# Performance work log

Measured on AMD Instinct MI355X. Metric: run time of the kernel, lower is better.

## Reference

```python
import jax, jax.numpy as jnp
import numpy as np

N, E, D_IN, D_OUT = 50000, 800000, 128, 128
LN_EPS = 1e-5


def setup_inputs() -> dict:
    key = jax.random.key(0)
    ks = jax.random.split(key, 7)
    x = jax.random.normal(ks[0], (N, D_IN), dtype=jnp.float32)
    adj = jax.random.randint(ks[1], (2, E), 0, N, dtype=jnp.int32)  # edge_index
    scale = 1.0 / np.sqrt(D_IN)
    W_gcn = jax.random.normal(ks[2], (D_IN, D_OUT), dtype=jnp.float32) * scale
    b_gcn = jax.random.normal(ks[3], (D_OUT,), dtype=jnp.float32) * 0.02
    W_lin = jax.random.normal(ks[4], (D_IN, D_OUT), dtype=jnp.float32) * scale
    ln_w = jnp.ones((D_OUT,), dtype=jnp.float32)
    ln_b = jnp.zeros((D_OUT,), dtype=jnp.float32)
    return {"adj": adj, "x": x, "W_gcn": W_gcn, "b_gcn": b_gcn,
            "W_lin": W_lin, "ln_w": ln_w, "ln_b": ln_b}


def _gcn_conv(x, edge_index, W, b):
    """PyG GCNConv: add self-loops, symmetric D^-1/2 (A+I) D^-1/2 normalization."""
    n = x.shape[0]
    loop = jnp.arange(n, dtype=edge_index.dtype)
    src = jnp.concatenate([edge_index[0], loop])  # message sources (x_j)
    dst = jnp.concatenate([edge_index[1], loop])  # aggregation targets
    ones = jnp.ones(src.shape[0], dtype=x.dtype)
    deg = jax.ops.segment_sum(ones, dst, num_segments=n)
    dinv = jnp.where(deg > 0, jax.lax.rsqrt(deg), 0.0)
    norm = dinv[src] * dinv[dst]                   # [E+N]
    h = x @ W                                      # [N, D_OUT] project first (PyG order)
    msg = h[src] * norm[:, None]                   # gather + scale
    agg = jax.ops.segment_sum(msg, dst, num_segments=n)
    return agg + b


def _layer_norm(y, w, b):
    mu = jnp.mean(y, axis=-1, keepdims=True)
    var = jnp.mean(jnp.square(y - mu), axis=-1, keepdims=True)
    return (y - mu) * jax.lax.rsqrt(var + LN_EPS) * w + b


def reference(adj, x, W_gcn, b_gcn, W_lin, ln_w, ln_b):
    x1 = _gcn_conv(x, adj, W_gcn, b_gcn)
    x2 = x @ W_lin                                  # bias=False linear
    return _layer_norm(x1 + x2 + 1e-6, ln_w, ln_b)
```

## Files before the change

kernel.cpp:

```cpp
#include <hip/hip_runtime.h>
#include <hip/hip_bf16.h>

#define NN 50000
#define EE 800000
#define DD 128
#define CB 196
#define EBLK 2048
#define NEB 391

typedef __attribute__((ext_vector_type(8))) short bf16x8;
typedef __attribute__((ext_vector_type(4))) float f32x4;

static __device__ __forceinline__ unsigned short f2bf(float f) {
  union { float f; unsigned u; } v; v.f = f;
  unsigned r = v.u + 0x7FFFu + ((v.u >> 16) & 1u);
  return (unsigned short)(r >> 16);
}
static __device__ __forceinline__ float bf2f(unsigned short h) {
  union { unsigned u; float f; } v; v.u = ((unsigned)h) << 16;
  return v.f;
}

__global__ __launch_bounds__(256) void k_p0(
    const int* __restrict__ dst, int* __restrict__ coarseCnt,
    const float* __restrict__ Wg, const float* __restrict__ Wl,
    unsigned short* __restrict__ Wt, const float4* __restrict__ x4,
    ushort4* __restrict__ xb4) {
  int b = blockIdx.x, t = threadIdx.x;
  if (b < NEB) {
    __shared__ int cnt[CB];
    for (int i = t; i < CB; i += 256) cnt[i] = 0;
    __syncthreads();
    int e0 = b * EBLK;
    for (int i = t; i < EBLK; i += 256) {
      int e = e0 + i;
      if (e < EE) atomicAdd(&cnt[dst[e] >> 8], 1);
    }
    __syncthreads();
    for (int i = t; i < CB; i += 256)
      if (cnt[i]) atomicAdd(&coarseCnt[i], cnt[i]);
  } else if (b < NEB + 32) {
    for (int i = (b - NEB) * 256 + t; i < DD * 256; i += 32 * 256) {
      int n = i >> 8, k = i & 255;
      float v = (k < 128) ? Wg[k * DD + n] : Wl[(k - 128) * DD + n];
      Wt[i] = f2bf(v);
    }
  } else {
    int base = (b - NEB - 32) * 1024 + t;
#pragma unroll
    for (int k = 0; k < 4; k++) {
      int i = base + k * 256;
      if (i < NN * 32) {
        float4 v = x4[i];
        ushort4 o;
        o.x = f2bf(v.x); o.y = f2bf(v.y); o.z = f2bf(v.z); o.w = f2bf(v.w);
        xb4[i] = o;
      }
    }
  }
}

__global__ __launch_bounds__(256) void k_pscan(const int* __restrict__ coarseCnt,
                                               int* __restrict__ coarseStart,
                                               int* __restrict__ cursor) {
  __shared__ int s[256];
  int t = threadIdx.x;
  int v = (t < CB) ? coarseCnt[t] : 0;
  s[t] = v;
  for (int off = 1; off < 256; off <<= 1) {
    __syncthreads();
    int tmp = (t >= off) ? s[t - off] : 0;
    __syncthreads();
    if (t >= off) s[t] += tmp;
  }
  __syncthreads();
  if (t < CB) {
    coarseStart[t] = s[t] - v;
    cursor[t] = s[t] - v;
  }
}

__global__ __launch_bounds__(256) void k_p1a(const int* __restrict__ src,
                                             const int* __restrict__ dst,
                                             int* __restrict__ cursor,
                                             unsigned int* __restrict__ pairs) {
  __shared__ unsigned int stage[EBLK];
  __shared__ int cnt[CB], base_[CB], cur[CB];
  int t = threadIdx.x;
  int e0 = blockIdx.x * EBLK;
  for (int i = t; i < CB; i += 256) { cnt[i] = 0; cur[i] = 0; }
  __syncthreads();
  for (int i = t; i < EBLK; i += 256) {
    int e = e0 + i;
    unsigned int p = 0xFFFFFFFFu;
    if (e < EE) {
      int d = dst[e], s = src[e];
      int cb = d >> 8;
      p = (unsigned int)s | ((unsigned int)(d & 255) << 16) | ((unsigned int)cb << 24);
      atomicAdd(&cnt[cb], 1);
    }
    stage[i] = p;
  }
  __syncthreads();
  for (int i = t; i < CB; i += 256)
    base_[i] = cnt[i] ? atomicAdd(&cursor[i], cnt[i]) : 0;
  __syncthreads();
  for (int i = t; i < EBLK; i += 256) {
    unsigned int p = stage[i];
    if (p != 0xFFFFFFFFu) {
      int cb = p >> 24;
      int ofs = atomicAdd(&cur[cb], 1);
      pairs[base_[cb] + ofs] = p;
    }
  }
}

__global__ __launch_bounds__(512) void k_p1b(
    const unsigned int* __restrict__ pairs, const int* __restrict__ coarseStart,
    const int* __restrict__ coarseCnt, const unsigned short* __restrict__ xb,
    int* __restrict__ deg, float* __restrict__ dinv, int* __restrict__ rowStart,
    unsigned short* __restrict__ srcU16, unsigned short* __restrict__ xs) {
  __shared__ int ldeg[256], lscan[256], lcur[256];
  __shared__ float ldinvs[256];
  int cb = blockIdx.x, t = threadIdx.x;
  int start = coarseStart[cb], cnt = coarseCnt[cb];
  int n0 = cb << 8;
  int nloc = NN - n0; if (nloc > 256) nloc = 256;
  if (t < 256) ldeg[t] = 0;
  __syncthreads();
  for (int i = t; i < cnt; i += 512)
    atomicAdd(&ldeg[(pairs[start + i] >> 16) & 255], 1);
  __syncthreads();
  if (t < 256) lscan[t] = ldeg[t];
  for (int off = 1; off < 256; off <<= 1) {
    __syncthreads();
    int tmp = (t >= off && t < 256) ? lscan[t - off] : 0;
    __syncthreads();
    if (t >= off && t < 256) lscan[t] += tmp;
  }
  __syncthreads();
  if (t < 256) {
    int dg = ldeg[t];
    int rs = start + lscan[t] - dg;
    lcur[t] = rs;
    float di = rsqrtf((float)(dg + 1));
    ldinvs[t] = di;
    if (t < nloc) { deg[n0 + t] = dg; dinv[n0 + t] = di; rowStart[n0 + t] = rs; }
  }
  __syncthreads();
  for (int i = t; i < cnt; i += 512) {
    unsigned int pr = pairs[start + i];
    int pos = atomicAdd(&lcur[(pr >> 16) & 255], 1);
    srcU16[pos] = (unsigned short)(pr & 0xFFFFu);
  }
  for (int i = t; i < nloc * 16; i += 512) {
    int rr = i >> 4, q = i & 15;
    bf16x8 v = *(const bf16x8*)(xb + (size_t)(n0 + rr) * DD + q * 8);
    float di = ldinvs[rr];
    bf16x8 o;
#pragma unroll
    for (int k = 0; k < 8; k++) o[k] = (short)f2bf(bf2f((unsigned short)v[k]) * di);
    *(bf16x8*)(xs + (size_t)(n0 + rr) * DD + q * 8) = o;
  }
}

__global__ __launch_bounds__(256) void k_agg2(
    const unsigned short* __restrict__ xs, const int* __restrict__ rowStart,
    const int* __restrict__ deg, const unsigned short* __restrict__ srcU16,
    const float* __restrict__ dinv, unsigned short* __restrict__ agg) {
  int t = threadIdx.x;
  int g = t >> 4, r = t & 15;
  int node = blockIdx.x * 16 + g;
  int lane = t & 63;
  int srcLaneBase = lane & 48;
  float acc[8];
  {
    bf16x8 vs = *(const bf16x8*)(xs + (size_t)node * DD + r * 8);
#pragma unroll
    for (int k = 0; k < 8; k++) acc[k] = bf2f((unsigned short)vs[k]);
  }
  int js = rowStart[node], cnt = deg[node];
  for (int base = 0; base < cnt; base += 16) {
    int idx = (base + r < cnt) ? (int)srcU16[js + base + r] : 0;
    int m = cnt - base; if (m > 16) m = 16;
    int j = 0;
    for (; j + 8 <= m; j += 8) {
      int s0 = __shfl(idx, srcLaneBase + j);
      int s1 = __shfl(idx, srcLaneBase + j + 1);
      int s2 = __shfl(idx, srcLaneBase + j + 2);
      int s3 = __shfl(idx, srcLaneBase + j + 3);
      int s4 = __shfl(idx, srcLaneBase + j + 4);
      int s5 = __shfl(idx, srcLaneBase + j + 5);
      int s6 = __shfl(idx, srcLaneBase + j + 6);
      int s7 = __shfl(idx, srcLaneBase + j + 7);
      bf16x8 v0 = *(const bf16x8*)(xs + (size_t)s0 * DD + r * 8);
      bf16x8 v1 = *(const bf16x8*)(xs + (size_t)s1 * DD + r * 8);
      bf16x8 v2 = *(const bf16x8*)(xs + (size_t)s2 * DD + r * 8);
      bf16x8 v3 = *(const bf16x8*)(xs + (size_t)s3 * DD + r * 8);
      bf16x8 v4 = *(const bf16x8*)(xs + (size_t)s4 * DD + r * 8);
      bf16x8 v5 = *(const bf16x8*)(xs + (size_t)s5 * DD + r * 8);
      bf16x8 v6 = *(const bf16x8*)(xs + (size_t)s6 * DD + r * 8);
      bf16x8 v7 = *(const bf16x8*)(xs + (size_t)s7 * DD + r * 8);
#pragma unroll
      for (int k = 0; k < 8; k++) acc[k] += bf2f((unsigned short)v0[k]);
#pragma unroll
      for (int k = 0; k < 8; k++) acc[k] += bf2f((unsigned short)v1[k]);
#pragma unroll
      for (int k = 0; k < 8; k++) acc[k] += bf2f((unsigned short)v2[k]);
#pragma unroll
      for (int k = 0; k < 8; k++) acc[k] += bf2f((unsigned short)v3[k]);
#pragma unroll
      for (int k = 0; k < 8; k++) acc[k] += bf2f((unsigned short)v4[k]);
#pragma unroll
      for (int k = 0; k < 8; k++) acc[k] += bf2f((unsigned short)v5[k]);
#pragma unroll
      for (int k = 0; k < 8; k++) acc[k] += bf2f((unsigned short)v6[k]);
#pragma unroll
      for (int k = 0; k < 8; k++) acc[k] += bf2f((unsigned short)v7[k]);
    }
    for (; j < m; j++) {
      int s = __shfl(idx, srcLaneBase + j);
      bf16x8 v = *(const bf16x8*)(xs + (size_t)s * DD + r * 8);
#pragma unroll
      for (int k = 0; k < 8; k++) acc[k] += bf2f((unsigned short)v[k]);
    }
  }
  float d = dinv[node];
  bf16x8 o;
#pragma unroll
  for (int k = 0; k < 8; k++) o[k] = (short)f2bf(acc[k] * d);
  *(bf16x8*)(agg + (size_t)node * DD + r * 8) = o;
}

__global__ __launch_bounds__(256) void k_mm_ln(
    const unsigned short* __restrict__ agg, const unsigned short* __restrict__ xb,
    const unsigned short* __restrict__ Wt, const float* __restrict__ bgcn,
    const float* __restrict__ lnw, const float* __restrict__ lnb,
    float* __restrict__ out) {
  int t = threadIdx.x;
  int w = t >> 6, lane = t & 63;
  int quad = lane >> 4, r = lane & 15;
  int m0 = (blockIdx.x * 4 + w) * 16;
  f32x4 zero = {0.f, 0.f, 0.f, 0.f};
  f32x4 acc[8];
#pragma unroll
  for (int i = 0; i < 8; i++) acc[i] = zero;
  int rowA = m0 + r;
  if (rowA > NN - 1) rowA = NN - 1;
#pragma unroll
  for (int ks = 0; ks < 8; ks++) {
    bf16x8 a;
    if (ks < 4) a = *(const bf16x8*)(agg + (size_t)rowA * DD + ks * 32 + quad * 8);
    else        a = *(const bf16x8*)(xb + (size_t)rowA * DD + (ks - 4) * 32 + quad * 8);
#pragma unroll
    for (int nt = 0; nt < 8; nt++) {
      bf16x8 b = *(const bf16x8*)(Wt + (size_t)(nt * 16 + r) * 256 + ks * 32 + quad * 8);
      acc[nt] = __builtin_amdgcn_mfma_f32_16x16x32_bf16(a, b, acc[nt], 0, 0, 0);
    }
  }
  float bg[8], lw[8], lb[8];
#pragma unroll
  for (int nt = 0; nt < 8; nt++) {
    int col = nt * 16 + r;
    bg[nt] = bgcn[col] + 1e-6f;
    lw[nt] = lnw[col];
    lb[nt] = lnb[col];
  }
#pragma unroll
  for (int reg = 0; reg < 4; reg++) {
    float y[8];
    float s1 = 0.f, s2 = 0.f;
#pragma unroll
    for (int nt = 0; nt < 8; nt++) {
      y[nt] = acc[nt][reg] + bg[nt];
      s1 += y[nt];
      s2 += y[nt] * y[nt];
    }
#pragma unroll
    for (int off = 1; off < 16; off <<= 1) {
      s1 += __shfl_xor(s1, off);
      s2 += __shfl_xor(s2, off);
    }
    float mu = s1 * (1.0f / 128.0f);
    float var = s2 * (1.0f / 128.0f) - mu * mu;
    float inv = rsqrtf(var + 1e-5f);
    int row = m0 + quad * 4 + reg;
    if (row < NN) {
#pragma unroll
      for (int nt = 0; nt < 8; nt++) {
        out[(size_t)row * DD + nt * 16 + r] = (y[nt] - mu) * inv * lw[nt] + lb[nt];
      }
    }
  }
}

extern "C" void kernel_launch(void* const* d_in, const int* in_sizes, int n_in,
                              void* d_out, int out_size, void* d_ws, size_t ws_size,
                              hipStream_t stream) {
  const int* adj = (const int*)d_in[0];
  const float* x = (const float*)d_in[1];
  const float* Wg = (const float*)d_in[2];
  const float* bg = (const float*)d_in[3];
  const float* Wl = (const float*)d_in[4];
  const float* lw = (const float*)d_in[5];
  const float* lb = (const float*)d_in[6];
  const int* srcp = adj;
  const int* dstp = adj + EE;
  float* out = (float*)d_out;

  char* ws = (char*)d_ws;
  size_t off = 0;
  auto alloc = [&](size_t bytes) -> void* {
    void* p = ws + off;
    off += (bytes + 255) & ~(size_t)255;
    return p;
  };
  int* coarseCnt = (int*)alloc((size_t)CB * 4);
  int* coarseStart = (int*)alloc((size_t)CB * 4);
  int* cursor = (int*)alloc((size_t)CB * 4);
  unsigned int* pairs = (unsigned int*)alloc((size_t)EE * 4);
  unsigned short* srcU16 = (unsigned short*)alloc((size_t)EE * 2);
  int* deg = (int*)alloc((size_t)NN * 4);
  float* dinv = (float*)alloc((size_t)NN * 4);
  int* rowStart = (int*)alloc((size_t)NN * 4);
  unsigned short* xb = (unsigned short*)alloc((size_t)NN * DD * 2);
  unsigned short* xs = (unsigned short*)alloc((size_t)NN * DD * 2);
  unsigned short* agg = (unsigned short*)alloc((size_t)NN * DD * 2);
  unsigned short* Wt = (unsigned short*)alloc((size_t)DD * 256 * 2);
  (void)ws_size; (void)in_sizes; (void)n_in; (void)out_size;

  hipMemsetAsync(coarseCnt, 0, (size_t)CB * 4, stream);
  k_p0<<<NEB + 32 + 1563, 256, 0, stream>>>(dstp, coarseCnt, Wg, Wl, Wt,
                                            (const float4*)x, (ushort4*)xb);
  k_pscan<<<1, 256, 0, stream>>>(coarseCnt, coarseStart, cursor);
  k_p1a<<<NEB, 256, 0, stream>>>(srcp, dstp, cursor, pairs);
  k_p1b<<<CB, 512, 0, stream>>>(pairs, coarseStart, coarseCnt, xb, deg, dinv,
                                rowStart, srcU16, xs);
  k_agg2<<<3125, 256, 0, stream>>>(xs, rowStart, deg, srcU16, dinv, agg);
  k_mm_ln<<<782, 256, 0, stream>>>(agg, xb, Wt, bg, lw, lb, out);
}
```

Before: 198.8 us.

## Fold coarse scan into partition kernels and count degrees with global atomics

Removes the single-block scan kernel. Each partition block now recomputes the coarse-bucket exclusive scan itself, and the per-node block derives its start offset from a reduction of earlier bucket counts. Node degrees are counted with global atomics in the first pass instead of a shared-memory histogram over pairs, and the edge block size is doubled to halve the block count. This saves one launch and a pass over pairs, at the cost of 800k global atomics on deg and redundant scans in every block.

```diff
diff --git a/kernel.cpp b/kernel.cpp
--- a/kernel.cpp
+++ b/kernel.cpp
@@ -5,8 +5,8 @@
 #define EE 800000
 #define DD 128
 #define CB 196
-#define EBLK 2048
-#define NEB 391
+#define EBLK 4096
+#define NEB 196
 
 typedef __attribute__((ext_vector_type(8))) short bf16x8;
 typedef __attribute__((ext_vector_type(4))) float f32x4;
@@ -23,6 +23,7 @@
 
 __global__ __launch_bounds__(256) void k_p0(
     const int* __restrict__ dst, int* __restrict__ coarseCnt,
+    int* __restrict__ deg,
     const float* __restrict__ Wg, const float* __restrict__ Wl,
     unsigned short* __restrict__ Wt, const float4* __restrict__ x4,
     ushort4* __restrict__ xb4) {
@@ -34,7 +35,11 @@
     int e0 = b * EBLK;
     for (int i = t; i < EBLK; i += 256) {
       int e = e0 + i;
-      if (e < EE) atomicAdd(&cnt[dst[e] >> 8], 1);
+      if (e < EE) {
+        int d = dst[e];
+        atomicAdd(&cnt[d >> 8], 1);
+        atomicAdd(&deg[d], 1);
+      }
     }
     __syncthreads();
     for (int i = t; i < CB; i += 256)
@@ -60,37 +65,21 @@
   }
 }
 
-__global__ __launch_bounds__(256) void k_pscan(const int* __restrict__ coarseCnt,
-                                               int* __restrict__ coarseStart,
-                                               int* __restrict__ cursor) {
-  __shared__ int s[256];
-  int t = threadIdx.x;
-  int v = (t < CB) ? coarseCnt[t] : 0;
-  s[t] = v;
-  for (int off = 1; off < 256; off <<= 1) {
-    __syncthreads();
-    int tmp = (t >= off) ? s[t - off] : 0;
-    __syncthreads();
-    if (t >= off) s[t] += tmp;
-  }
-  __syncthreads();
-  if (t < CB) {
-    coarseStart[t] = s[t] - v;
-    cursor[t] = s[t] - v;
-  }
-}
-
-__global__ __launch_bounds__(256) void k_p1a(const int* __restrict__ src,
+__global__ __launch_bounds__(512) void k_p1a(const int* __restrict__ src,
                                              const int* __restrict__ dst,
-                                             int* __restrict__ cursor,
+                                             const int* __restrict__ coarseCnt,
+                                             int* __restrict__ cursor0,
                                              unsigned int* __restrict__ pairs) {
   __shared__ unsigned int stage[EBLK];
-  __shared__ int cnt[CB], base_[CB], cur[CB];
+  __shared__ int sc[256];
+  __shared__ int cnt[CB], rb[CB], cur[CB];
   int t = threadIdx.x;
   int e0 = blockIdx.x * EBLK;
-  for (int i = t; i < CB; i += 256) { cnt[i] = 0; cur[i] = 0; }
-  __syncthreads();
-  for (int i = t; i < EBLK; i += 256) {
+  int own = 0;
+  if (t < CB) { cnt[t] = 0; cur[t] = 0; }
+  if (t < 256) { own = (t < CB) ? coarseCnt[t] : 0; sc[t] = own; }
+  __syncthreads();
+  for (int i = t; i < EBLK; i += 512) {
     int e = e0 + i;
     unsigned int p = 0xFFFFFFFFu;
     if (e < EE) {
@@ -101,51 +90,65 @@
     }
     stage[i] = p;
   }
-  __syncthreads();
-  for (int i = t; i < CB; i += 256)
-    base_[i] = cnt[i] ? atomicAdd(&cursor[i], cnt[i]) : 0;
-  __syncthreads();
-  for (int i = t; i < EBLK; i += 256) {
+  for (int off = 1; off < 256; off <<= 1) {
+    __syncthreads();
+    int tmp = (t < 256 && t >= off) ? sc[t - off] : 0;
+    __syncthreads();
+    if (t < 256 && t >= off) sc[t] += tmp;
+  }
+  __syncthreads();
+  if (t < CB) {
+    int excl = sc[t] - own;
+    rb[t] = excl + (cnt[t] ? atomicAdd(&cursor0[t], cnt[t]) : 0);
+  }
+  __syncthreads();
+  for (int i = t; i < EBLK; i += 512) {
     unsigned int p = stage[i];
     if (p != 0xFFFFFFFFu) {
       int cb = p >> 24;
       int ofs = atomicAdd(&cur[cb], 1);
-      pairs[base_[cb] + ofs] = p;
+      pairs[rb[cb] + ofs] = p;
     }
   }
 }
 
 __global__ __launch_bounds__(512) void k_p1b(
-    const unsigned int* __restrict__ pairs, const int* __restrict__ coarseStart,
-    const int* __restrict__ coarseCnt, const unsigned short* __restrict__ xb,
-    int* __restrict__ deg, float* __restrict__ dinv, int* __restrict__ rowStart,
+    const unsigned int* __restrict__ pairs, const int* __restrict__ coarseCnt,
+    const int* __restrict__ deg, const unsigned short* __restrict__ xb,
+    float* __restrict__ dinv, int* __restrict__ rowStart,
     unsigned short* __restrict__ srcU16, unsigned short* __restrict__ xs) {
-  __shared__ int ldeg[256], lscan[256], lcur[256];
+  __shared__ int sc[256], lcur[256];
   __shared__ float ldinvs[256];
-  int cb = blockIdx.x, t = threadIdx.x;
-  int start = coarseStart[cb], cnt = coarseCnt[cb];
-  int n0 = cb << 8;
+  __shared__ int wsum[8];
+  int b = blockIdx.x, t = threadIdx.x;
+  int n0 = b << 8;
   int nloc = NN - n0; if (nloc > 256) nloc = 256;
-  if (t < 256) ldeg[t] = 0;
-  __syncthreads();
-  for (int i = t; i < cnt; i += 512)
-    atomicAdd(&ldeg[(pairs[start + i] >> 16) & 255], 1);
-  __syncthreads();
-  if (t < 256) lscan[t] = ldeg[t];
+  int partial = 0;
+  for (int i = t; i < b; i += 512) partial += coarseCnt[i];
+#pragma unroll
+  for (int off = 32; off > 0; off >>= 1) partial += __shfl_xor(partial, off);
+  if ((t & 63) == 0) wsum[t >> 6] = partial;
+  int dg = 0;
+  if (t < 256) {
+    dg = (t < nloc) ? deg[n0 + t] : 0;
+    sc[t] = dg;
+  }
   for (int off = 1; off < 256; off <<= 1) {
     __syncthreads();
-    int tmp = (t >= off && t < 256) ? lscan[t - off] : 0;
-    __syncthreads();
-    if (t >= off && t < 256) lscan[t] += tmp;
-  }
-  __syncthreads();
+    int tmp = (t < 256 && t >= off) ? sc[t - off] : 0;
+    __syncthreads();
+    if (t < 256 && t >= off) sc[t] += tmp;
+  }
+  __syncthreads();
+  int start = wsum[0] + wsum[1] + wsum[2] + wsum[3] +
+              wsum[4] + wsum[5] + wsum[6] + wsum[7];
+  int cnt = sc[255];
   if (t < 256) {
-    int dg = ldeg[t];
-    int rs = start + lscan[t] - dg;
+    int rs = start + sc[t] - dg;
     lcur[t] = rs;
     float di = rsqrtf((float)(dg + 1));
     ldinvs[t] = di;
-    if (t < nloc) { deg[n0 + t] = dg; dinv[n0 + t] = di; rowStart[n0 + t] = rs; }
+    if (t < nloc) { rowStart[n0 + t] = rs; dinv[n0 + t] = di; }
   }
   __syncthreads();
   for (int i = t; i < cnt; i += 512) {
@@ -315,12 +318,12 @@
     off += (bytes + 255) & ~(size_t)255;
     return p;
   };
-  int* coarseCnt = (int*)alloc((size_t)CB * 4);
-  int* coarseStart = (int*)alloc((size_t)CB * 4);
-  int* cursor = (int*)alloc((size_t)CB * 4);
+  int* zb = (int*)alloc((size_t)(256 + 256 + NN) * 4);
+  int* coarseCnt = zb;
+  int* cursor0 = zb + 256;
+  int* deg = zb + 512;
   unsigned int* pairs = (unsigned int*)alloc((size_t)EE * 4);
   unsigned short* srcU16 = (unsigned short*)alloc((size_t)EE * 2);
-  int* deg = (int*)alloc((size_t)NN * 4);
   float* dinv = (float*)alloc((size_t)NN * 4);
   int* rowStart = (int*)alloc((size_t)NN * 4);
   unsigned short* xb = (unsigned short*)alloc((size_t)NN * DD * 2);
@@ -329,13 +332,12 @@
   unsigned short* Wt = (unsigned short*)alloc((size_t)DD * 256 * 2);
   (void)ws_size; (void)in_sizes; (void)n_in; (void)out_size;
 
-  hipMemsetAsync(coarseCnt, 0, (size_t)CB * 4, stream);
-  k_p0<<<NEB + 32 + 1563, 256, 0, stream>>>(dstp, coarseCnt, Wg, Wl, Wt,
+  hipMemsetAsync(zb, 0, (size_t)(512 + NN) * 4, stream);
+  k_p0<<<NEB + 32 + 1563, 256, 0, stream>>>(dstp, coarseCnt, deg, Wg, Wl, Wt,
                                             (const float4*)x, (ushort4*)xb);
-  k_pscan<<<1, 256, 0, stream>>>(coarseCnt, coarseStart, cursor);
-  k_p1a<<<NEB, 256, 0, stream>>>(srcp, dstp, cursor, pairs);
-  k_p1b<<<CB, 512, 0, stream>>>(pairs, coarseStart, coarseCnt, xb, deg, dinv,
-                                rowStart, srcU16, xs);
+  k_p1a<<<NEB, 512, 0, stream>>>(srcp, dstp, coarseCnt, cursor0, pairs);
+  k_p1b<<<CB, 512, 0, stream>>>(pairs, coarseCnt, deg, xb, dinv, rowStart,
+                                srcU16, xs);
   k_agg2<<<3125, 256, 0, stream>>>(xs, rowStart, deg, srcU16, dinv, agg);
   k_mm_ln<<<782, 256, 0, stream>>>(agg, xb, Wt, bg, lw, lb, out);
 }
```

Result: slower. 217.8 us (+9.6%).
